# Kernel tuning notes

Hardware: AMD Instinct MI355X
Metric: run time of the kernel (lower is better)

Reference implementation:

```python
import jax, jax.numpy as jnp
import numpy as np

NUM_TAGS = 32  # 30 real tags + START + STOP
START = 30
STOP = 31
B = 1024
S = 512


def setup_inputs() -> dict:
    key = jax.random.key(0)
    k1, k2, k3, k4 = jax.random.split(key, 4)
    feats = jax.random.normal(k1, (B, S, NUM_TAGS), dtype=jnp.float32)
    labels = jax.random.randint(k2, (B, S), 0, START, dtype=jnp.int32)
    lengths = jax.random.randint(k3, (B,), 1, S + 1, dtype=jnp.int32)
    transitions = jax.random.normal(k4, (NUM_TAGS, NUM_TAGS), dtype=jnp.float32)
    # replicate CRF.__init__: no transition INTO START, none OUT of STOP
    transitions = transitions.at[:, START].set(-10000.0)
    transitions = transitions.at[STOP, :].set(-10000.0)
    return {"feats": feats, "labels": labels, "lengths": lengths, "transitions": transitions}


def reference(feats, labels, lengths, transitions):
    # Original torch code uses self.transitions.data (detached) everywhere,
    # so transitions receive no gradient -> stop_gradient for faithfulness.
    trans = jax.lax.stop_gradient(transitions)
    Bn, Sn, T = feats.shape

    # ---- log-partition (CRF.forward), batched over B with masked scan ----
    alpha0 = feats[:, 0, :] + trans[START][None, :]  # [B,T]

    def step(alpha, inp):
        feat_t, t = inp  # feat_t: [B,T]
        # scores[b,i,j] = alpha[b,i] + trans[i,j] + feat_t[b,j]
        scores = alpha[:, :, None] + trans[None, :, :] + feat_t[:, None, :]
        new_alpha = jax.nn.logsumexp(scores, axis=1)  # [B,T]
        alpha = jnp.where((t < lengths)[:, None], new_alpha, alpha)
        return alpha, None

    feats_t = jnp.swapaxes(feats[:, 1:, :], 0, 1)  # [S-1,B,T]
    alpha, _ = jax.lax.scan(step, alpha0, (feats_t, jnp.arange(1, Sn)))
    # NOTE: original forward omits the STOP transition (only logsumexp) -> replicate
    forward_score = jax.nn.logsumexp(alpha, axis=1)  # [B]

    # ---- gold score (CRF.gold_score), fully vectorized ----
    pos = jnp.arange(Sn)[None, :]  # [1,S]
    valid = pos < lengths[:, None]  # [B,S]
    emit = jnp.take_along_axis(feats, labels[:, :, None].astype(jnp.int32), axis=2)[:, :, 0]
    emit_sum = jnp.sum(jnp.where(valid, emit, 0.0), axis=1)
    start_sc = trans[START, labels[:, 0]]
    pair = trans[labels[:, :-1], labels[:, 1:]]  # [B,S-1]
    pair_sum = jnp.sum(jnp.where(valid[:, 1:], pair, 0.0), axis=1)
    last_tag = jnp.take_along_axis(labels, (lengths - 1)[:, None], axis=1)[:, 0]
    stop_sc = trans[last_tag, STOP]
    gold_score = emit_sum + start_sc + pair_sum + stop_sc  # [B]

    return jnp.sum(forward_score - gold_score) / Bn
```

## Files before the change

kernel.cpp:

```cpp
#include <hip/hip_runtime.h>
#include <math.h>


constexpr int NTAG = 32;
constexpr int TSTART = 30;
constexpr int TSTOP = 31;
constexpr int NB = 1024;
constexpr int NS = 512;

constexpr float LOG2E = 1.44269504088896340736f;
constexpr float LN2   = 0.69314718055994530942f;

typedef float v2f __attribute__((ext_vector_type(2)));
typedef unsigned int v2u __attribute__((ext_vector_type(2)));

__device__ __forceinline__ float fexp2(float x) {
#if __has_builtin(__builtin_amdgcn_exp2f)
    return __builtin_amdgcn_exp2f(x);
#else
    return exp2f(x);
#endif
}

__device__ __forceinline__ v2f pk_mul(v2f a, v2f b) {
    v2f d;
    asm("v_pk_mul_f32 %0, %1, %2" : "=v"(d) : "v"(a), "v"(b));
    return d;
}
__device__ __forceinline__ v2f pk_fma(v2f a, v2f b, v2f c) {
    v2f d;
    asm("v_pk_fma_f32 %0, %1, %2, %3" : "=v"(d) : "v"(a), "v"(b), "v"(c));
    return d;
}
__device__ __forceinline__ v2f pk_add(v2f a, v2f b) {
    v2f d;
    asm("v_pk_add_f32 %0, %1, %2" : "=v"(d) : "v"(a), "v"(b));
    return d;
}

__device__ __forceinline__ float swap32_partner(float v) {
#if __has_builtin(__builtin_amdgcn_permlane32_swap)
    v2u r = __builtin_amdgcn_permlane32_swap(
        __float_as_uint(v), __float_as_uint(v), false, false);
    return (__uint_as_float(r.x) + __uint_as_float(r.y)) - v;
#else
    unsigned a = __float_as_uint(v), b = a;
    asm("s_nop 1\n\tv_permlane32_swap_b32 %0, %1" : "+v"(a), "+v"(b));
    return (__uint_as_float(a) + __uint_as_float(b)) - v;
#endif
}

__global__ __launch_bounds__(64)
void crf_fwd(const float* __restrict__ feats,
             const int*   __restrict__ labels,
             const int*   __restrict__ lengths,
             const float* __restrict__ trans,
             float*       __restrict__ out)
{
    const int j   = threadIdx.x;
    const int j32 = j & 31;
    const int b   = blockIdx.x;

    const int hs = (j & 32) >> 1;
    const int dl = j32 ^ hs;

    v2f EO[8], ET[8];
    #pragma unroll
    for (int k = 0; k < 8; ++k) {
        int n0 = 2 * k, n1 = 2 * k + 1;
        int s0 = ((j32 & 16) | ((j32 - n0) & 15)) ^ hs;
        int s1 = ((j32 & 16) | ((j32 - n1) & 15)) ^ hs;
        EO[k].x = fexp2(trans[(s0 << 5) + dl] * LOG2E);
        EO[k].y = fexp2(trans[(s1 << 5) + dl] * LOG2E);
        ET[k].x = fexp2(trans[(s0 << 5) + (dl ^ 16)] * LOG2E);
        ET[k].y = fexp2(trans[(s1 << 5) + (dl ^ 16)] * LOG2E);
    }

    const int len = lengths[b];
    const float* fb = feats  + (size_t)b * NS * NTAG;
    const int*   lb = labels + (size_t)b * NS;

    int labr[8];
    #pragma unroll
    for (int k = 0; k < 8; ++k)
        labr[k] = lb[(k << 6) + j];

    float x = fexp2((fb[dl] + trans[(TSTART << 5) + dl]) * LOG2E);

    int bits0 = __builtin_amdgcn_readfirstlane(__float_as_int(x));
    int e0    = min(max((bits0 >> 23) & 0xFF, 1), 254);
    int kreg  = e0 - 127;
    int creg  = 0;

    float pf[8];
    #pragma unroll
    for (int u = 0; u < 8; ++u) {
        int tt = min(1 + u, NS - 1);
        pf[u] = fb[(size_t)tt * NTAG + dl];
    }

    const int nsteps = len - 1;
    const int nchunk = nsteps >> 3;
    const int rem    = nsteps & 7;
    int t = 1;

    #define RORV(SRC, N) __int_as_float(__builtin_amdgcn_update_dpp(          \
        0, __float_as_int(SRC), 0x120 + (N), 0xF, 0xF, false))

    #define CRF_STEP(FEAT, RN)                                                \
    {                                                                         \
        float F_;                                                             \
        if (RN) {                                                             \
            creg += kreg;                                                     \
            F_ = fexp2(fmaf((FEAT), LOG2E, -(float)kreg));                    \
        } else {                                                              \
            F_ = fexp2((FEAT) * LOG2E);                                       \
        }                                                                     \
        float x1 = RORV(x, 1),  x2 = RORV(x, 2),  x3 = RORV(x, 3);            \
        float x4 = RORV(x, 4),  x5 = RORV(x, 5),  x6 = RORV(x, 6);            \
        float x7 = RORV(x, 7),  x8 = RORV(x, 8),  x9 = RORV(x, 9);            \
        float x10 = RORV(x, 10), x11 = RORV(x, 11), x12 = RORV(x, 12);        \
        float x13 = RORV(x, 13), x14 = RORV(x, 14), x15 = RORV(x, 15);        \
        v2f R0; R0.x = x;   R0.y = x1;                                        \
        v2f R1; R1.x = x2;  R1.y = x3;                                        \
        v2f R2; R2.x = x4;  R2.y = x5;                                        \
        v2f R3; R3.x = x6;  R3.y = x7;                                        \
        v2f R4; R4.x = x8;  R4.y = x9;                                        \
        v2f R5; R5.x = x10; R5.y = x11;                                       \
        v2f R6; R6.x = x12; R6.y = x13;                                       \
        v2f R7; R7.x = x14; R7.y = x15;                                       \
        v2f a0 = pk_mul(R0, EO[0]);                                           \
        v2f b0 = pk_mul(R0, ET[0]);                                           \
        v2f a1 = pk_mul(R1, EO[1]);                                           \
        v2f b1 = pk_mul(R1, ET[1]);                                           \
        a0 = pk_fma(R2, EO[2], a0);  b0 = pk_fma(R2, ET[2], b0);              \
        a1 = pk_fma(R3, EO[3], a1);  b1 = pk_fma(R3, ET[3], b1);              \
        a0 = pk_fma(R4, EO[4], a0);  b0 = pk_fma(R4, ET[4], b0);              \
        a1 = pk_fma(R5, EO[5], a1);  b1 = pk_fma(R5, ET[5], b1);              \
        a0 = pk_fma(R6, EO[6], a0);  b0 = pk_fma(R6, ET[6], b0);              \
        a1 = pk_fma(R7, EO[7], a1);  b1 = pk_fma(R7, ET[7], b1);              \
        v2f va = pk_add(a0, a1);                                              \
        v2f vb = pk_add(b0, b1);                                              \
        float accOwn = va.x + va.y;                                           \
        float accOth = vb.x + vb.y;                                           \
        float qv = accOwn + swap32_partner(accOth);                           \
        x = qv * F_;                                                          \
        if (RN) {                                                             \
            int bits_ = __builtin_amdgcn_readfirstlane(__float_as_int(x));    \
            int e_ = min(max((bits_ >> 23) & 0xFF, 1), 254);                  \
            kreg = e_ - 127;                                                  \
        }                                                                     \
    }

    for (int ci = 0; ci < nchunk; ++ci) {
        #pragma unroll
        for (int u = 0; u < 8; ++u) {
            float feat = pf[u];
            int   tp   = min(t + 8, NS - 1);
            pf[u] = fb[(size_t)tp * NTAG + dl];
            if (u & 1) { CRF_STEP(feat, 1) }
            else       { CRF_STEP(feat, 0) }
            ++t;
        }
    }
    #pragma unroll
    for (int u = 0; u < 7; ++u) {
        if (u < rem) {
            if (u & 1) { CRF_STEP(pf[u], 1) }
            else       { CRF_STEP(pf[u], 0) }
            ++t;
        }
    }
    #undef CRF_STEP
    #undef RORV

    float s = x;
    #pragma unroll
    for (int m = 1; m <= 16; m <<= 1)
        s += __shfl_xor(s, m, 64);
    float fwd = (float)creg * LN2 + logf(s);

    float gold = 0.0f;
    #pragma unroll
    for (int k = 0; k < 8; ++k) {
        int tt = (k << 6) + j;
        if (tt < len) {
            int lab_t = labr[k];
            gold += fb[(size_t)tt * NTAG + lab_t];
            if (tt > 0)
                gold += trans[(lb[tt - 1] << 5) + lab_t];
            else
                gold += trans[(TSTART << 5) + lab_t];
            if (tt == len - 1)
                gold += trans[(lab_t << 5) + TSTOP];
        }
    }
    #pragma unroll
    for (int m = 1; m <= 32; m <<= 1)
        gold += __shfl_xor(gold, m, 64);

    if (j == 0)
        atomicAdd(out, (fwd - gold) * (1.0f / 1024.0f));
}

extern "C" void kernel_launch(void* const* d_in, const int* in_sizes, int n_in,
                              void* d_out, int out_size, void* d_ws, size_t ws_size,
                              hipStream_t stream) {
    const float* feats   = (const float*)d_in[0];
    const int*   labels  = (const int*)d_in[1];
    const int*   lengths = (const int*)d_in[2];
    const float* trans   = (const float*)d_in[3];
    float*       out     = (float*)d_out;

    hipMemsetAsync(out, 0, sizeof(float) * (size_t)out_size, stream);
    crf_fwd<<<dim3(NB), dim3(64), 0, stream>>>(feats, labels, lengths, trans, out);
}
```

Measured before the change: 163.6 us.

## Split CRF step into alternating 16/32-lane partial sums with half the FMAs

Reorganizes how the 32x32 transition product is split across the 64 lanes. Each lane now keeps one 16-term partial product per step instead of two, and even and odd steps alternate between a permlane16 swap and a permlane32 swap to combine partials. This roughly halves the packed FMA work per serial step on the critical recurrence path. In exchange the lane-to-tag mapping rotates between steps, the final reduction now covers both 32-lane halves and subtracts ln2 for the duplicated state, and the s_nop before the inline-asm permlane swap is removed, which could cause a hazard if the builtin is unavailable.

```diff
diff --git a/kernel.cpp b/kernel.cpp
--- a/kernel.cpp
+++ b/kernel.cpp
@@ -45,7 +45,18 @@
     return (__uint_as_float(r.x) + __uint_as_float(r.y)) - v;
 #else
     unsigned a = __float_as_uint(v), b = a;
-    asm("s_nop 1\n\tv_permlane32_swap_b32 %0, %1" : "+v"(a), "+v"(b));
+    asm("v_permlane32_swap_b32 %0, %1" : "+v"(a), "+v"(b));
+    return (__uint_as_float(a) + __uint_as_float(b)) - v;
+#endif
+}
+__device__ __forceinline__ float swap16_partner(float v) {
+#if __has_builtin(__builtin_amdgcn_permlane16_swap)
+    v2u r = __builtin_amdgcn_permlane16_swap(
+        __float_as_uint(v), __float_as_uint(v), false, false);
+    return (__uint_as_float(r.x) + __uint_as_float(r.y)) - v;
+#else
+    unsigned a = __float_as_uint(v), b = a;
+    asm("v_permlane16_swap_b32 %0, %1" : "+v"(a), "+v"(b));
     return (__uint_as_float(a) + __uint_as_float(b)) - v;
 #endif
 }
@@ -61,19 +72,19 @@
     const int j32 = j & 31;
     const int b   = blockIdx.x;
 
-    const int hs = (j & 32) >> 1;
-    const int dl = j32 ^ hs;
-
-    v2f EO[8], ET[8];
+    const int i  = j & 15;
+    const int c1 = j & 16;
+    const int c2 = (j & 32) >> 1;
+
+    v2f Tm[8], Ts[8];
     #pragma unroll
     for (int k = 0; k < 8; ++k) {
         int n0 = 2 * k, n1 = 2 * k + 1;
-        int s0 = ((j32 & 16) | ((j32 - n0) & 15)) ^ hs;
-        int s1 = ((j32 & 16) | ((j32 - n1) & 15)) ^ hs;
-        EO[k].x = fexp2(trans[(s0 << 5) + dl] * LOG2E);
-        EO[k].y = fexp2(trans[(s1 << 5) + dl] * LOG2E);
-        ET[k].x = fexp2(trans[(s0 << 5) + (dl ^ 16)] * LOG2E);
-        ET[k].y = fexp2(trans[(s1 << 5) + (dl ^ 16)] * LOG2E);
+        int a0s = ((i - n0) & 15), a1s = ((i - n1) & 15);
+        Tm[k].x = fexp2(trans[((a0s | c1) << 5) + (i | c2)] * LOG2E);
+        Tm[k].y = fexp2(trans[((a1s | c1) << 5) + (i | c2)] * LOG2E);
+        Ts[k].x = fexp2(trans[((a0s | c2) << 5) + (i | c1)] * LOG2E);
+        Ts[k].y = fexp2(trans[((a1s | c2) << 5) + (i | c1)] * LOG2E);
     }
 
     const int len = lengths[b];
@@ -85,7 +96,10 @@
     for (int k = 0; k < 8; ++k)
         labr[k] = lb[(k << 6) + j];
 
-    float x = fexp2((fb[dl] + trans[(TSTART << 5) + dl]) * LOG2E);
+    const int fxA = i | c2;
+    const int fxB = j32;
+
+    float x = fexp2((fb[j32] + trans[(TSTART << 5) + j32]) * LOG2E);
 
     int bits0 = __builtin_amdgcn_readfirstlane(__float_as_int(x));
     int e0    = min(max((bits0 >> 23) & 0xFF, 1), 254);
@@ -96,7 +110,7 @@
     #pragma unroll
     for (int u = 0; u < 8; ++u) {
         int tt = min(1 + u, NS - 1);
-        pf[u] = fb[(size_t)tt * NTAG + dl];
+        pf[u] = fb[(size_t)tt * NTAG + ((u & 1) ? fxB : fxA)];
     }
 
     const int nsteps = len - 1;
@@ -107,7 +121,7 @@
     #define RORV(SRC, N) __int_as_float(__builtin_amdgcn_update_dpp(          \
         0, __float_as_int(SRC), 0x120 + (N), 0xF, 0xF, false))
 
-    #define CRF_STEP(FEAT, RN)                                                \
+    #define CRF_STEP(FEAT, TBL, SW, RN)                                       \
     {                                                                         \
         float F_;                                                             \
         if (RN) {                                                             \
@@ -129,22 +143,18 @@
         v2f R5; R5.x = x10; R5.y = x11;                                       \
         v2f R6; R6.x = x12; R6.y = x13;                                       \
         v2f R7; R7.x = x14; R7.y = x15;                                       \
-        v2f a0 = pk_mul(R0, EO[0]);                                           \
-        v2f b0 = pk_mul(R0, ET[0]);                                           \
-        v2f a1 = pk_mul(R1, EO[1]);                                           \
-        v2f b1 = pk_mul(R1, ET[1]);                                           \
-        a0 = pk_fma(R2, EO[2], a0);  b0 = pk_fma(R2, ET[2], b0);              \
-        a1 = pk_fma(R3, EO[3], a1);  b1 = pk_fma(R3, ET[3], b1);              \
-        a0 = pk_fma(R4, EO[4], a0);  b0 = pk_fma(R4, ET[4], b0);              \
-        a1 = pk_fma(R5, EO[5], a1);  b1 = pk_fma(R5, ET[5], b1);              \
-        a0 = pk_fma(R6, EO[6], a0);  b0 = pk_fma(R6, ET[6], b0);              \
-        a1 = pk_fma(R7, EO[7], a1);  b1 = pk_fma(R7, ET[7], b1);              \
+        v2f a0 = pk_mul(R0, TBL[0]);                                          \
+        v2f a1 = pk_mul(R1, TBL[1]);                                          \
+        a0 = pk_fma(R2, TBL[2], a0);                                          \
+        a1 = pk_fma(R3, TBL[3], a1);                                          \
+        a0 = pk_fma(R4, TBL[4], a0);                                          \
+        a1 = pk_fma(R5, TBL[5], a1);                                          \
+        a0 = pk_fma(R6, TBL[6], a0);                                          \
+        a1 = pk_fma(R7, TBL[7], a1);                                          \
         v2f va = pk_add(a0, a1);                                              \
-        v2f vb = pk_add(b0, b1);                                              \
-        float accOwn = va.x + va.y;                                           \
-        float accOth = vb.x + vb.y;                                           \
-        float qv = accOwn + swap32_partner(accOth);                           \
-        x = qv * F_;                                                          \
+        float own = va.x + va.y;                                              \
+        float part = (SW == 16) ? swap16_partner(own) : swap32_partner(own);  \
+        x = (own + part) * F_;                                                \
         if (RN) {                                                             \
             int bits_ = __builtin_amdgcn_readfirstlane(__float_as_int(x));    \
             int e_ = min(max((bits_ >> 23) & 0xFF, 1), 254);                  \
@@ -157,17 +167,17 @@
         for (int u = 0; u < 8; ++u) {
             float feat = pf[u];
             int   tp   = min(t + 8, NS - 1);
-            pf[u] = fb[(size_t)tp * NTAG + dl];
-            if (u & 1) { CRF_STEP(feat, 1) }
-            else       { CRF_STEP(feat, 0) }
+            pf[u] = fb[(size_t)tp * NTAG + ((u & 1) ? fxB : fxA)];
+            if (u & 1) { CRF_STEP(feat, Ts, 32, 1) }
+            else       { CRF_STEP(feat, Tm, 16, 0) }
             ++t;
         }
     }
     #pragma unroll
     for (int u = 0; u < 7; ++u) {
         if (u < rem) {
-            if (u & 1) { CRF_STEP(pf[u], 1) }
-            else       { CRF_STEP(pf[u], 0) }
+            if (u & 1) { CRF_STEP(pf[u], Ts, 32, 1) }
+            else       { CRF_STEP(pf[u], Tm, 16, 0) }
             ++t;
         }
     }
@@ -176,9 +186,9 @@
 
     float s = x;
     #pragma unroll
-    for (int m = 1; m <= 16; m <<= 1)
+    for (int m = 1; m <= 32; m <<= 1)
         s += __shfl_xor(s, m, 64);
-    float fwd = (float)creg * LN2 + logf(s);
+    float fwd = (float)creg * LN2 + logf(s) - LN2;
 
     float gold = 0.0f;
     #pragma unroll
```

Measured after the change: 152.8 us. 1.07x faster.
